# Optimization experiments

Hardware: AMD Instinct MI355X
Metric: run time of the kernel (lower is better)

The kernel has to match this reference:

```python
import jax, jax.numpy as jnp
import numpy as np


def _binarize_kernel_wise(w):
    # Bi-ViT LinearBi (Qmodes.kernel_wise): per-output-channel scale alpha = mean(|w|)
    # quantized weight w_q = alpha * sign(w).  w: [out, in]
    alpha = jnp.mean(jnp.abs(w), axis=1, keepdims=True)  # [out, 1]
    return alpha * jnp.sign(w)


def setup_inputs() -> dict:
    key = jax.random.key(0)
    k_x, k_w1, k_b1, k_w2, k_b2 = jax.random.split(key, 5)
    B, N, C, H = 64, 197, 768, 3072
    x = jax.random.normal(k_x, (B, N, C), dtype=jnp.float32)
    w1 = jax.random.normal(k_w1, (H, C), dtype=jnp.float32) * 0.02
    b1 = jax.random.normal(k_b1, (H,), dtype=jnp.float32) * 0.02
    w2 = jax.random.normal(k_w2, (C, H), dtype=jnp.float32) * 0.02
    b2 = jax.random.normal(k_b2, (C,), dtype=jnp.float32) * 0.02
    return {"x": x, "w1": w1, "b1": b1, "w2": w2, "b2": b2}


def reference(x, w1, b1, w2, b2):
    # fc1 (binarized linear, kernel-wise scales)
    w1_q = _binarize_kernel_wise(w1)
    h = jnp.einsum('bnc,hc->bnh', x, w1_q) + b1
    # GELU (exact, erf-based as torch nn.GELU default) then clip to [-10, 10]
    h = jnp.clip(jax.nn.gelu(h, approximate=False), -10.0, 10.0)
    # dropout p=0.0 -> identity
    w2_q = _binarize_kernel_wise(w2)
    out = jnp.einsum('bnh,ch->bnc', h, w2_q) + b2
    return out
```

## Files before the change

kernel.cpp:

```cpp
#include <hip/hip_runtime.h>
#include <hip/hip_bf16.h>
#include <cstdint>
#include <cstddef>


typedef __bf16 bf16x8 __attribute__((ext_vector_type(8)));
typedef __bf16 bf16x4 __attribute__((ext_vector_type(4)));
typedef float floatx4 __attribute__((ext_vector_type(4)));

__device__ __forceinline__ void async_load16(const void* g, void* l) {
    __builtin_amdgcn_global_load_lds(
        (const __attribute__((address_space(1))) void*)g,
        (__attribute__((address_space(3))) void*)l,
        16, 0, 0);
}

__global__ __launch_bounds__(256) void x_to_bf16(
    const float* __restrict__ in, __hip_bfloat16* __restrict__ out, int n4)
{
    int i = blockIdx.x * 256 + threadIdx.x;
    if (i < n4) {
        float4 v = ((const float4*)in)[i];
        bf16x4 o;
        o[0] = (__bf16)v.x; o[1] = (__bf16)v.y;
        o[2] = (__bf16)v.z; o[3] = (__bf16)v.w;
        ((bf16x4*)out)[i] = o;
    }
}

__global__ __launch_bounds__(256) void bin_prep(
    const float* __restrict__ w,
    __hip_bfloat16* __restrict__ sgn,
    float* __restrict__ alpha,
    int cols4)
{
    const int row = blockIdx.x;
    const float4* wr = (const float4*)w + (size_t)row * cols4;
    bf16x4* sr = (bf16x4*)sgn + (size_t)row * cols4;
    float s = 0.0f;
    for (int c = threadIdx.x; c < cols4; c += 256) {
        float4 v = wr[c];
        s += fabsf(v.x) + fabsf(v.y) + fabsf(v.z) + fabsf(v.w);
        bf16x4 o;
        o[0] = (__bf16)(v.x > 0.0f ? 1.0f : (v.x < 0.0f ? -1.0f : 0.0f));
        o[1] = (__bf16)(v.y > 0.0f ? 1.0f : (v.y < 0.0f ? -1.0f : 0.0f));
        o[2] = (__bf16)(v.z > 0.0f ? 1.0f : (v.z < 0.0f ? -1.0f : 0.0f));
        o[3] = (__bf16)(v.w > 0.0f ? 1.0f : (v.w < 0.0f ? -1.0f : 0.0f));
        sr[c] = o;
    }
    #pragma unroll
    for (int off = 32; off > 0; off >>= 1) s += __shfl_down(s, off, 64);
    __shared__ float wsum[4];
    const int lane = threadIdx.x & 63;
    const int wv = threadIdx.x >> 6;
    if (lane == 0) wsum[wv] = s;
    __syncthreads();
    if (threadIdx.x == 0) {
        float t = wsum[0] + wsum[1] + wsum[2] + wsum[3];
        alpha[row] = t / (float)(cols4 * 4);
    }
}

#define TILE_M 128
#define TILE_N 128
#define TILE_K 64

__device__ __forceinline__ void store_val(__hip_bfloat16* C, size_t idx, float v) {
    C[idx] = __float2bfloat16(v);
}
__device__ __forceinline__ void store_val(float* C, size_t idx, float v) {
    C[idx] = v;
}

template <bool DO_GELU, typename OutT>
__global__ __launch_bounds__(256) void gemm_bin(
    const __hip_bfloat16* __restrict__ A,
    const __hip_bfloat16* __restrict__ S,
    const float* __restrict__ alpha,
    const float* __restrict__ bias,
    OutT* __restrict__ C,
    int M, int N, int K)
{
    __shared__ __align__(16) __hip_bfloat16 sA[TILE_M * TILE_K];
    __shared__ __align__(16) __hip_bfloat16 sB[TILE_N * TILE_K];

    const int tid = threadIdx.x;
    const int wave = tid >> 6;
    const int lane = tid & 63;
    const int bm = blockIdx.y * TILE_M;
    const int bn = blockIdx.x * TILE_N;

    const int wm = (wave & 1) * 64;
    const int wn = (wave >> 1) * 64;
    const int lr = lane & 15;
    const int kq = lane >> 4;
    const int e3 = lr & 7;

    const int crow = lane >> 3;
    const int ccol = (((lane & 7) ^ crow) * 8);

    floatx4 acc[4][4];
    #pragma unroll
    for (int i = 0; i < 4; i++)
        #pragma unroll
        for (int j = 0; j < 4; j++)
            #pragma unroll
            for (int r = 0; r < 4; r++)
                acc[i][j][r] = 0.0f;

    for (int k0 = 0; k0 < K; k0 += TILE_K) {
        #pragma unroll
        for (int j = 0; j < 4; j++) {
            const int seg = wave * 4 + j;
            const int r = seg * 8 + crow;
            int ar = bm + r;
            ar = ar < M ? ar : (M - 1);
            async_load16(A + (size_t)ar * K + (k0 + ccol), (void*)(sA + seg * 512));
            async_load16(S + (size_t)(bn + r) * K + (k0 + ccol), (void*)(sB + seg * 512));
        }
        __syncthreads();

        #pragma unroll
        for (int ks = 0; ks < 2; ks++) {
            const int slot = ((ks << 2) | kq) ^ e3;
            bf16x8 af[4], bfv[4];
            #pragma unroll
            for (int i = 0; i < 4; i++)
                af[i] = *(const bf16x8*)(sA + (wm + i * 16 + lr) * TILE_K + slot * 8);
            #pragma unroll
            for (int j = 0; j < 4; j++)
                bfv[j] = *(const bf16x8*)(sB + (wn + j * 16 + lr) * TILE_K + slot * 8);
            #pragma unroll
            for (int i = 0; i < 4; i++)
                #pragma unroll
                for (int j = 0; j < 4; j++)
                    acc[i][j] = __builtin_amdgcn_mfma_f32_16x16x32_bf16(
                        af[i], bfv[j], acc[i][j], 0, 0, 0);
        }
        __syncthreads();
    }

    float al[4], bi[4];
    #pragma unroll
    for (int j = 0; j < 4; j++) {
        const int col = bn + wn + j * 16 + lr;
        al[j] = alpha[col];
        bi[j] = bias[col];
    }
    #pragma unroll
    for (int i = 0; i < 4; i++) {
        const int row0 = bm + wm + i * 16 + (lane >> 4) * 4;
        #pragma unroll
        for (int r = 0; r < 4; r++) {
            const int row = row0 + r;
            if (row < M) {
                #pragma unroll
                for (int j = 0; j < 4; j++) {
                    float v = acc[i][j][r] * al[j] + bi[j];
                    if (DO_GELU) {
                        v = 0.5f * v * (1.0f + erff(v * 0.70710678118654752f));
                        v = fminf(fmaxf(v, -10.0f), 10.0f);
                    }
                    store_val(C, (size_t)row * N + (bn + wn + j * 16 + lr), v);
                }
            }
        }
    }
}

extern "C" void kernel_launch(void* const* d_in, const int* in_sizes, int n_in,
                              void* d_out, int out_size, void* d_ws, size_t ws_size,
                              hipStream_t stream) {
    const float* x  = (const float*)d_in[0];
    const float* w1 = (const float*)d_in[1];
    const float* b1 = (const float*)d_in[2];
    const float* w2 = (const float*)d_in[3];
    const float* b2 = (const float*)d_in[4];

    const int M = 64 * 197;
    const int Cd = 768;
    const int Hd = 3072;

    char* ws = (char*)d_ws;
    __hip_bfloat16* xb   = (__hip_bfloat16*)ws;
    __hip_bfloat16* sgn1 = xb + (size_t)M * Cd;
    __hip_bfloat16* sgn2 = sgn1 + (size_t)Hd * Cd;
    float* alpha1 = (float*)(sgn2 + (size_t)Cd * Hd);
    float* alpha2 = alpha1 + Hd;
    __hip_bfloat16* hbuf = (__hip_bfloat16*)(alpha2 + Cd);

    const int n4 = (M * Cd) / 4;
    x_to_bf16<<<(n4 + 255) / 256, 256, 0, stream>>>(x, xb, n4);
    bin_prep<<<Hd, 256, 0, stream>>>(w1, sgn1, alpha1, Cd / 4);
    bin_prep<<<Cd, 256, 0, stream>>>(w2, sgn2, alpha2, Hd / 4);

    const int gm = (M + TILE_M - 1) / TILE_M;
    gemm_bin<true,  __hip_bfloat16><<<dim3(Hd / TILE_N, gm), 256, 0, stream>>>(
        xb, sgn1, alpha1, b1, hbuf, M, Hd, Cd);
    gemm_bin<false, float><<<dim3(Cd / TILE_N, gm), 256, 0, stream>>>(
        hbuf, sgn2, alpha2, b2, (float*)d_out, M, Cd, Hd);
}
```

Before: 283.0 us.

## Switch GEMMs to 32x32x16 MFMA and use 64-row tiles for second GEMM

Replaces the 16x16x32 bf16 MFMA tiling with 32x32x16 MFMA, so each wave computes 2x2 (or 1x2) 32x32 blocks with 16-wide accumulators. This changes the LDS fragment reads and the epilogue row mapping. The GEMM is templated on tile M, and the second GEMM (N=768) uses 64-row tiles to double its block count and improve CU occupancy. The larger MFMA shape cuts LDS reads per FLOP, while the smaller tile for GEMM2 gives less reuse per block. M/64 divides exactly (12608/64=197).

```diff
diff --git a/kernel.cpp b/kernel.cpp
--- a/kernel.cpp
+++ b/kernel.cpp
@@ -6,7 +6,7 @@
 
 typedef __bf16 bf16x8 __attribute__((ext_vector_type(8)));
 typedef __bf16 bf16x4 __attribute__((ext_vector_type(4)));
-typedef float floatx4 __attribute__((ext_vector_type(4)));
+typedef float floatx16 __attribute__((ext_vector_type(16)));
 
 __device__ __forceinline__ void async_load16(const void* g, void* l) {
     __builtin_amdgcn_global_load_lds(
@@ -61,10 +61,6 @@
     }
 }
 
-#define TILE_M 128
-#define TILE_N 128
-#define TILE_K 64
-
 __device__ __forceinline__ void store_val(__hip_bfloat16* C, size_t idx, float v) {
     C[idx] = __float2bfloat16(v);
 }
@@ -72,7 +68,7 @@
     C[idx] = v;
 }
 
-template <bool DO_GELU, typename OutT>
+template <int TM, bool DO_GELU, typename OutT>
 __global__ __launch_bounds__(256) void gemm_bin(
     const __hip_bfloat16* __restrict__ A,
     const __hip_bfloat16* __restrict__ S,
@@ -81,87 +77,99 @@
     OutT* __restrict__ C,
     int M, int N, int K)
 {
-    __shared__ __align__(16) __hip_bfloat16 sA[TILE_M * TILE_K];
-    __shared__ __align__(16) __hip_bfloat16 sB[TILE_N * TILE_K];
+    constexpr int TN = 128;
+    constexpr int TK = 64;
+    constexpr int ASEG = TM / 8;
+    constexpr int RSEG = ASEG + TN / 8;
+    constexpr int PW   = RSEG / 4;
+    constexpr int WMT  = TM / 2;
+    constexpr int MI   = WMT / 32;
+
+    __shared__ __align__(16) __hip_bfloat16 sA[TM * TK];
+    __shared__ __align__(16) __hip_bfloat16 sB[TN * TK];
 
     const int tid = threadIdx.x;
     const int wave = tid >> 6;
     const int lane = tid & 63;
-    const int bm = blockIdx.y * TILE_M;
-    const int bn = blockIdx.x * TILE_N;
-
-    const int wm = (wave & 1) * 64;
+    const int bm = blockIdx.y * TM;
+    const int bn = blockIdx.x * TN;
+
+    const int wm = (wave & 1) * WMT;
     const int wn = (wave >> 1) * 64;
-    const int lr = lane & 15;
-    const int kq = lane >> 4;
-    const int e3 = lr & 7;
+    const int ln = lane & 31;
+    const int kh = lane >> 5;
+    const int e3 = lane & 7;
 
     const int crow = lane >> 3;
-    const int ccol = (((lane & 7) ^ crow) * 8);
-
-    floatx4 acc[4][4];
-    #pragma unroll
-    for (int i = 0; i < 4; i++)
-        #pragma unroll
-        for (int j = 0; j < 4; j++)
-            #pragma unroll
-            for (int r = 0; r < 4; r++)
+    const int ccol = ((lane & 7) ^ crow) * 8;
+
+    floatx16 acc[MI][2];
+    #pragma unroll
+    for (int i = 0; i < MI; i++)
+        #pragma unroll
+        for (int j = 0; j < 2; j++)
+            #pragma unroll
+            for (int r = 0; r < 16; r++)
                 acc[i][j][r] = 0.0f;
 
-    for (int k0 = 0; k0 < K; k0 += TILE_K) {
-        #pragma unroll
-        for (int j = 0; j < 4; j++) {
-            const int seg = wave * 4 + j;
-            const int r = seg * 8 + crow;
-            int ar = bm + r;
-            ar = ar < M ? ar : (M - 1);
-            async_load16(A + (size_t)ar * K + (k0 + ccol), (void*)(sA + seg * 512));
-            async_load16(S + (size_t)(bn + r) * K + (k0 + ccol), (void*)(sB + seg * 512));
+    for (int k0 = 0; k0 < K; k0 += TK) {
+        #pragma unroll
+        for (int t = 0; t < PW; t++) {
+            const int seg = wave * PW + t;
+            if (seg < ASEG) {
+                const int r = seg * 8 + crow;
+                int ar = bm + r;
+                ar = ar < M ? ar : (M - 1);
+                async_load16(A + (size_t)ar * K + (k0 + ccol), (void*)(sA + seg * 512));
+            } else {
+                const int r = (seg - ASEG) * 8 + crow;
+                async_load16(S + (size_t)(bn + r) * K + (k0 + ccol),
+                             (void*)(sB + (seg - ASEG) * 512));
+            }
         }
         __syncthreads();
 
         #pragma unroll
-        for (int ks = 0; ks < 2; ks++) {
-            const int slot = ((ks << 2) | kq) ^ e3;
-            bf16x8 af[4], bfv[4];
-            #pragma unroll
-            for (int i = 0; i < 4; i++)
-                af[i] = *(const bf16x8*)(sA + (wm + i * 16 + lr) * TILE_K + slot * 8);
-            #pragma unroll
-            for (int j = 0; j < 4; j++)
-                bfv[j] = *(const bf16x8*)(sB + (wn + j * 16 + lr) * TILE_K + slot * 8);
-            #pragma unroll
-            for (int i = 0; i < 4; i++)
+        for (int ks = 0; ks < 4; ks++) {
+            const int slot = ((ks * 2 + kh) ^ e3) * 8;
+            bf16x8 af[MI], bfv[2];
+            #pragma unroll
+            for (int i = 0; i < MI; i++)
+                af[i] = *(const bf16x8*)(sA + (wm + i * 32 + ln) * TK + slot);
+            #pragma unroll
+            for (int j = 0; j < 2; j++)
+                bfv[j] = *(const bf16x8*)(sB + (wn + j * 32 + ln) * TK + slot);
+            #pragma unroll
+            for (int i = 0; i < MI; i++)
                 #pragma unroll
-                for (int j = 0; j < 4; j++)
-                    acc[i][j] = __builtin_amdgcn_mfma_f32_16x16x32_bf16(
+                for (int j = 0; j < 2; j++)
+                    acc[i][j] = __builtin_amdgcn_mfma_f32_32x32x16_bf16(
                         af[i], bfv[j], acc[i][j], 0, 0, 0);
         }
         __syncthreads();
     }
 
-    float al[4], bi[4];
-    #pragma unroll
-    for (int j = 0; j < 4; j++) {
-        const int col = bn + wn + j * 16 + lr;
+    float al[2], bi[2];
+    #pragma unroll
+    for (int j = 0; j < 2; j++) {
+        const int col = bn + wn + j * 32 + ln;
         al[j] = alpha[col];
         bi[j] = bias[col];
     }
     #pragma unroll
-    for (int i = 0; i < 4; i++) {
-        const int row0 = bm + wm + i * 16 + (lane >> 4) * 4;
-        #pragma unroll
-        for (int r = 0; r < 4; r++) {
-            const int row = row0 + r;
+    for (int i = 0; i < MI; i++) {
+        #pragma unroll
+        for (int r = 0; r < 16; r++) {
+            const int row = bm + wm + i * 32 + (r & 3) + 8 * (r >> 2) + 4 * kh;
             if (row < M) {
                 #pragma unroll
-                for (int j = 0; j < 4; j++) {
+                for (int j = 0; j < 2; j++) {
                     float v = acc[i][j][r] * al[j] + bi[j];
                     if (DO_GELU) {
                         v = 0.5f * v * (1.0f + erff(v * 0.70710678118654752f));
                         v = fminf(fmaxf(v, -10.0f), 10.0f);
                     }
-                    store_val(C, (size_t)row * N + (bn + wn + j * 16 + lr), v);
+                    store_val(C, (size_t)row * N + (bn + wn + j * 32 + ln), v);
                 }
             }
         }
@@ -194,9 +202,10 @@
     bin_prep<<<Hd, 256, 0, stream>>>(w1, sgn1, alpha1, Cd / 4);
     bin_prep<<<Cd, 256, 0, stream>>>(w2, sgn2, alpha2, Hd / 4);
 
-    const int gm = (M + TILE_M - 1) / TILE_M;
-    gemm_bin<true,  __hip_bfloat16><<<dim3(Hd / TILE_N, gm), 256, 0, stream>>>(
+    gemm_bin<128, true, __hip_bfloat16>
+        <<<dim3(Hd / 128, (M + 127) / 128), 256, 0, stream>>>(
         xb, sgn1, alpha1, b1, hbuf, M, Hd, Cd);
-    gemm_bin<false, float><<<dim3(Cd / TILE_N, gm), 256, 0, stream>>>(
+    gemm_bin<64, false, float>
+        <<<dim3(Cd / 128, M / 64), 256, 0, stream>>>(
         hbuf, sgn2, alpha2, b2, (float*)d_out, M, Cd, Hd);
 }
```

Measured after the change: 295.9 us. 4.6% more time.
